# Optimization experiments

Hardware: AMD Instinct MI355X
Metric: run time of the kernel (lower is better)

Reference implementation:

```python
import jax, jax.numpy as jnp
import numpy as np

D_MODEL = 2048
N_HEAD = 16
N_KV_HEAD = 4
D_HEAD = D_MODEL // N_HEAD  # 128
WINDOW = 512
B, T = 2, 2048


def _rope_tables(T, d_head, base=10000.0):
    inv = 1.0 / (base ** (np.arange(0, d_head, 2, dtype=np.float32) / d_head))
    t = np.arange(T, dtype=np.float32)
    freqs = np.outer(t, inv)  # [T, d_head//2]
    return jnp.asarray(np.cos(freqs)), jnp.asarray(np.sin(freqs))


def setup_inputs() -> dict:
    key = jax.random.key(0)
    ks = jax.random.split(key, 5)
    cos, sin = _rope_tables(T, D_HEAD)
    s = 1.0 / np.sqrt(D_MODEL)
    return {
        "x": jax.random.normal(ks[0], (B, T, D_MODEL), jnp.float32),
        "cos": cos,
        "sin": sin,
        "Wq": jax.random.normal(ks[1], (D_MODEL, D_MODEL), jnp.float32) * s,
        "Wk": jax.random.normal(ks[2], (D_MODEL, N_KV_HEAD * D_HEAD), jnp.float32) * s,
        "Wv": jax.random.normal(ks[3], (D_MODEL, N_KV_HEAD * D_HEAD), jnp.float32) * s,
        "Wo": jax.random.normal(ks[4], (D_MODEL, D_MODEL), jnp.float32) * s,
    }


def _apply_rope(t, cos, sin):
    # t: [B, T, H, D]; cos/sin: [T, D//2]; interleaved-pair (complex) rotation
    tr = t[..., 0::2]
    ti = t[..., 1::2]
    c = cos[None, :, None, :]
    s = sin[None, :, None, :]
    out_r = tr * c - ti * s
    out_i = tr * s + ti * c
    return jnp.stack([out_r, out_i], axis=-1).reshape(t.shape)


def reference(x, cos, sin, Wq, Wk, Wv, Wo):
    Bx, Tx, C = x.shape
    q = (x @ Wq).reshape(Bx, Tx, N_HEAD, D_HEAD)       # [B,T,H,D]
    k = (x @ Wk).reshape(Bx, Tx, N_KV_HEAD, D_HEAD)    # [B,T,Hkv,D]
    v = (x @ Wv).reshape(Bx, Tx, N_KV_HEAD, D_HEAD)
    q = _apply_rope(q, cos, sin)
    k = _apply_rope(k, cos, sin)
    n_rep = N_HEAD // N_KV_HEAD
    k = jnp.repeat(k, n_rep, axis=2)  # [B,T,H,D]
    v = jnp.repeat(v, n_rep, axis=2)
    scale = 1.0 / np.sqrt(D_HEAD)
    att = jnp.einsum("bihd,bjhd->bhij", q, k) * scale  # [B,H,T,T]
    i = jnp.arange(Tx)[:, None]
    j = jnp.arange(Tx)[None, :]
    mask = (j <= i) & (j >= i - WINDOW + 1)            # causal sliding window
    att = jnp.where(mask[None, None], att, -jnp.inf)
    att = jax.nn.softmax(att, axis=-1)
    y = jnp.einsum("bhij,bjhd->bihd", att, v).reshape(Bx, Tx, C)
    return y @ Wo
```

## Files before the change

### kernel.cpp

```cpp
#include <hip/hip_runtime.h>
#include <hip/hip_bf16.h>
#include <cstdint>
#include <cstddef>

#define B_ 2
#define T_ 2048
#define NH 16
#define NKV 4
#define DH 128
#define DM 2048
#define WIN 512
#define QKS 2560

typedef __attribute__((ext_vector_type(4))) float f32x4;
typedef __attribute__((ext_vector_type(8))) __bf16 bf16x8;

using bf16 = __hip_bfloat16;

__device__ inline void gload_lds16(const void* g, void* l) {
  __builtin_amdgcn_global_load_lds(
      (const __attribute__((address_space(1))) void*)g,
      (__attribute__((address_space(3))) void*)l, 16, 0, 0);
}

__device__ inline unsigned pack_bf2(float a, float b) {
  unsigned short ua = __builtin_bit_cast(unsigned short, __float2bfloat16(a));
  unsigned short ub = __builtin_bit_cast(unsigned short, __float2bfloat16(b));
  return (unsigned)ua | ((unsigned)ub << 16);
}

#define FBAR()                           \
  do {                                   \
    asm volatile("" ::: "memory");       \
    __builtin_amdgcn_s_barrier();        \
    asm volatile("" ::: "memory");       \
  } while (0)

__global__ __launch_bounds__(256) void k_prep(const float* __restrict__ x,
                                              const float* __restrict__ Wq,
                                              const float* __restrict__ Wk,
                                              const float* __restrict__ Wv,
                                              const float* __restrict__ Wo,
                                              bf16* __restrict__ xb,
                                              bf16* __restrict__ Wqkvt,
                                              bf16* __restrict__ Wot) {
  int id = blockIdx.x;
  int tid = threadIdx.x;
  if (id >= 2560) {
    size_t base = (size_t)(id - 2560) * 4096 + tid * 16;
#pragma unroll
    for (int j = 0; j < 4; ++j) {
      float4 v = *(const float4*)(x + base + j * 4);
      ushort4 o;
      o.x = __builtin_bit_cast(unsigned short, __float2bfloat16(v.x));
      o.y = __builtin_bit_cast(unsigned short, __float2bfloat16(v.y));
      o.z = __builtin_bit_cast(unsigned short, __float2bfloat16(v.z));
      o.w = __builtin_bit_cast(unsigned short, __float2bfloat16(v.w));
      *(ushort4*)(xb + base + j * 4) = o;
    }
    return;
  }
  const float* W;
  bf16* Wt;
  int N, bx, by;
  if (id < 1024) { W = Wq; Wt = Wqkvt; N = 2048; bx = id & 31; by = id >> 5; }
  else if (id < 1280) { id -= 1024; W = Wk; Wt = Wqkvt + (size_t)2048 * 2048; N = 512; bx = id & 7; by = id >> 3; }
  else if (id < 1536) { id -= 1280; W = Wv; Wt = Wqkvt + (size_t)2560 * 2048; N = 512; bx = id & 7; by = id >> 3; }
  else { id -= 1536; W = Wo; Wt = Wot; N = 2048; bx = id & 31; by = id >> 5; }

  __shared__ float tile[64][65];
  int n0 = bx * 64, k0 = by * 64;
  int tx = tid & 63, tg = tid >> 6;
#pragma unroll
  for (int r = 0; r < 16; ++r) {
    int k = tg * 16 + r;
    tile[k][tx] = W[(size_t)(k0 + k) * N + n0 + tx];
  }
  __syncthreads();
#pragma unroll
  for (int r = 0; r < 16; ++r) {
    int nn = tg * 16 + r;
    Wt[(size_t)(n0 + nn) * 2048 + k0 + tx] = __float2bfloat16(tile[tx][nn]);
  }
}

template <int BN, int EPI>
__global__ __launch_bounds__(512, 2) void k_gemm2(const bf16* __restrict__ A,
                                                  const bf16* __restrict__ Bt,
                                                  void* __restrict__ Cout,
                                                  int M, int N, int K,
                                                  const float* __restrict__ cosT,
                                                  const float* __restrict__ sinT,
                                                  bf16* __restrict__ vt) {
  constexpr int NR = BN / 32;
  constexpr int NB = BN * 128 / 8192;
  __shared__ __align__(16) char As_[2][32768];
  __shared__ __align__(16) char Bs_[2][BN * 128];

  const int tid = threadIdx.x;
  const int w = tid >> 6, lane = tid & 63;
  const int li = lane & 15, g = lane >> 4;
  const int wm = w >> 1, wn = w & 1;

  const int nwg = gridDim.x * gridDim.y;
  int bid = blockIdx.y * gridDim.x + blockIdx.x;
  bid = (bid & 7) * (nwg >> 3) + (bid >> 3);
  const int m0 = (bid / gridDim.x) * 256;
  const int n0 = (bid % gridDim.x) * BN;

  const int ntiles = K >> 6;

  auto sA = [&](int buf, int tile, int h, int issue) {
    if (tile >= ntiles) return;
    const int rl = issue * 64 + (tid >> 3);
    const int row = (rl >> 5) * 64 + h * 32 + (rl & 31);
    const int sl = tid & 7;
    const bf16* src = A + (size_t)(m0 + row) * K + tile * 64 + ((sl ^ (rl & 7)) * 8);
    gload_lds16(src, As_[buf] + h * 16384 + issue * 8192 + tid * 16);
  };
  auto sB = [&](int buf, int tile, int issue) {
    if (tile >= ntiles) return;
    const int block = issue * 8 + w;
    const int rr = block * 8 + (lane >> 3);
    const int sl = lane & 7;
    const bf16* src = Bt + (size_t)(n0 + rr) * K + tile * 64 + ((sl ^ (rr & 7)) * 8);
    gload_lds16(src, Bs_[buf] + block * 1024);
  };

  const int swz0 = (g ^ (li & 7)) * 16;
  const int swz1 = ((4 + g) ^ (li & 7)) * 16;
  bf16x8 af[4], bv[NR * 2];
  f32x4 acc[4][NR] = {};

  auto readA = [&](int buf, int mh) {
#pragma unroll
    for (int m2 = 0; m2 < 2; ++m2) {
      const int rl = wm * 32 + m2 * 16 + li;
      const char* p = As_[buf] + mh * 16384 + rl * 128;
      af[m2 * 2 + 0] = *(const bf16x8*)(p + swz0);
      af[m2 * 2 + 1] = *(const bf16x8*)(p + swz1);
    }
  };
  auto readB = [&](int buf) {
#pragma unroll
    for (int n = 0; n < NR; ++n) {
      const char* p = Bs_[buf] + (wn * (NR * 16) + n * 16 + li) * 128;
      bv[n * 2 + 0] = *(const bf16x8*)(p + swz0);
      bv[n * 2 + 1] = *(const bf16x8*)(p + swz1);
    }
  };
  auto MMA = [&](int mh) {
    __builtin_amdgcn_s_setprio(1);
#pragma unroll
    for (int m2 = 0; m2 < 2; ++m2)
#pragma unroll
      for (int n = 0; n < NR; ++n)
#pragma unroll
        for (int kk = 0; kk < 2; ++kk)
          acc[mh * 2 + m2][n] = __builtin_amdgcn_mfma_f32_16x16x32_bf16(
              af[m2 * 2 + kk], bv[n * 2 + kk], acc[mh * 2 + m2][n], 0, 0, 0);
    __builtin_amdgcn_s_setprio(0);
  };

  sA(0, 0, 0, 0); sA(0, 0, 0, 1);
#pragma unroll
  for (int i = 0; i < NB; ++i) sB(0, 0, i);
  sA(0, 0, 1, 0); sA(0, 0, 1, 1);
  asm volatile("s_waitcnt vmcnt(2)" ::: "memory");
  __builtin_amdgcn_sched_barrier(0);
  FBAR();

  for (int t = 0; t < ntiles; ++t) {
    const int cb = t & 1;
    const bool last = (t == ntiles - 1);
    readA(cb, 0); readB(cb);
    sA(cb ^ 1, t + 1, 0, 0); sA(cb ^ 1, t + 1, 0, 1);
#pragma unroll
    for (int i = 0; i < NB; ++i) sB(cb ^ 1, t + 1, i);
    if (last) {
      asm volatile("s_waitcnt vmcnt(0)" ::: "memory");
    } else if constexpr (NB == 3) {
      asm volatile("s_waitcnt vmcnt(5)" ::: "memory");
    } else {
      asm volatile("s_waitcnt vmcnt(4)" ::: "memory");
    }
    __builtin_amdgcn_sched_barrier(0);
    FBAR(); MMA(0); FBAR();
    readA(cb, 1);
    sA(cb ^ 1, t + 1, 1, 0); sA(cb ^ 1, t + 1, 1, 1);
    if (last)
      asm volatile("s_waitcnt vmcnt(0)" ::: "memory");
    else
      asm volatile("s_waitcnt vmcnt(2)" ::: "memory");
    __builtin_amdgcn_sched_barrier(0);
    FBAR(); MMA(1); FBAR();
  }

#pragma unroll
  for (int mf = 0; mf < 4; ++mf)
#pragma unroll
    for (int nf = 0; nf < NR; ++nf) {
      const int colc = n0 + wn * (NR * 16) + nf * 16;
      const int col = colc + li;
      const int row0 = m0 + wm * 64 + mf * 16 + g * 4;
      if constexpr (EPI == 2) {
        if (colc < QKS) {
          const float qs = (colc < 2048) ? 0.08838834764831845f : 1.0f;
          const int i = (col & 127) >> 1;
          const float sgn = (li & 1) ? 1.0f : -1.0f;
#pragma unroll
          for (int r = 0; r < 4; ++r) {
            const int trow = (row0 + r) & (T_ - 1);
            float v = acc[mf][nf][r];
            float pv = __shfl_xor(v, 1);
            float c = cosT[trow * 64 + i], s = sinT[trow * 64 + i];
            float o = (v * c + pv * (sgn * s)) * qs;
            ((bf16*)Cout)[(size_t)(row0 + r) * QKS + col] = __float2bfloat16(o);
          }
        } else {
          unsigned lo = pack_bf2(acc[mf][nf][0], acc[mf][nf][1]);
          unsigned hi = pack_bf2(acc[mf][nf][2], acc[mf][nf][3]);
          uint2 pk = {lo, hi};
          *(uint2*)(vt + (size_t)(col - QKS) * (B_ * T_) + row0) = pk;
        }
      } else {
#pragma unroll
        for (int r = 0; r < 4; ++r)
          ((float*)Cout)[(size_t)(row0 + r) * N + col] = acc[mf][nf][r];
      }
    }
}

__global__ __launch_bounds__(512, 2) void k_attn(const bf16* __restrict__ qkv,
                                                 const bf16* __restrict__ vt,
                                                 bf16* __restrict__ Y) {
  __shared__ __align__(16) char Ks[2][9216];
  __shared__ __align__(16) char Vs[2][10240];
  __shared__ __align__(16) char Pl[8][2][1280];
  const int lane = threadIdx.x & 63;
  const int w = threadIdx.x >> 6;
  const int li = lane & 15, g = lane >> 4;
  const int t0 = ((int)gridDim.x - 1 - (int)blockIdx.x) * 64;
  const int b = blockIdx.y / NKV, kvh = blockIdx.y % NKV;
  const int h = kvh * 4 + (w >> 1);
  const int qrow0 = t0 + (w & 1) * 32;

  bf16x8 qf[2][4];
#pragma unroll
  for (int s = 0; s < 2; ++s) {
    const bf16* qbase = qkv + (size_t)(b * T_ + qrow0 + s * 16 + li) * QKS + h * DH;
#pragma unroll
    for (int dk = 0; dk < 4; ++dk) qf[s][dk] = *(const bf16x8*)(qbase + dk * 32 + g * 8);
  }

  float mrow[2] = {-1e4f, -1e4f};
  float srow[2] = {0.f, 0.f};
  f32x4 acc[2][8] = {};

  int ks0 = t0 - (WIN - 1);
  if (ks0 < 0) ks0 = 0;
  ks0 &= ~31;
  const int nt = (t0 + 63 - ks0) / 32 + 1;

  const bf16* kgbase = qkv + (size_t)(b * T_) * QKS + DM + kvh * DH;
  const bf16* vgbase = vt + (size_t)(kvh * DH) * (B_ * T_) + b * T_;

  auto STAGE = [&](int buf, int kt) {
    for (int c = w; c < 19; c += 8) {
      if (c < 9) {
        int slot = c * 64 + lane;
        int row = slot / 17, cc = slot % 17;
        if (slot >= 544) { row = 0; cc = 0; }
        if (cc == 16) cc = 0;
        const bf16* src = kgbase + (size_t)(kt + row) * QKS + cc * 8;
        gload_lds16(src, Ks[buf] + c * 1024);
      } else {
        int c2 = c - 9;
        int slot = c2 * 64 + lane;
        int row = slot / 5, cc = slot % 5;
        if (cc == 4) cc = 0;
        const bf16* src = vgbase + (size_t)row * (B_ * T_) + kt + cc * 8;
        gload_lds16(src, Vs[buf] + c2 * 1024);
      }
    }
  };

  STAGE(0, ks0);
  __syncthreads();
  int cur = 0;

  for (int it = 0; it < nt; ++it) {
    const int kt = ks0 + it * 32;
    if (it + 1 < nt) STAGE(cur ^ 1, kt + 32);

    if (!(kt > qrow0 + 31 || kt + 31 < qrow0 - (WIN - 1))) {
      f32x4 sc[2][2] = {};
#pragma unroll
      for (int n = 0; n < 2; ++n)
#pragma unroll
        for (int dk = 0; dk < 4; ++dk) {
          bf16x8 kf = *(const bf16x8*)(Ks[cur] + (n * 16 + li) * 272 + dk * 64 + g * 16);
          sc[0][n] = __builtin_amdgcn_mfma_f32_16x16x32_bf16(kf, qf[0][dk], sc[0][n], 0, 0, 0);
          sc[1][n] = __builtin_amdgcn_mfma_f32_16x16x32_bf16(kf, qf[1][dk], sc[1][n], 0, 0, 0);
        }

#pragma unroll
      for (int s = 0; s < 2; ++s) {
        const int t = qrow0 + s * 16 + li;
        float p[2][4];
        float pmax = -1e30f;
#pragma unroll
        for (int n = 0; n < 2; ++n)
#pragma unroll
          for (int r = 0; r < 4; ++r) {
            int key = kt + n * 16 + g * 4 + r;
            bool valid = (key <= t) && (key > t - WIN);
            float pv = valid ? sc[s][n][r] : -1e30f;
            p[n][r] = pv;
            pmax = fmaxf(pmax, pv);
          }
        pmax = fmaxf(pmax, __shfl_xor(pmax, 16));
        pmax = fmaxf(pmax, __shfl_xor(pmax, 32));

        if (!__all(pmax <= mrow[s])) {
          float nm = fmaxf(mrow[s], pmax);
          float alpha = __expf(mrow[s] - nm);
          mrow[s] = nm;
          srow[s] *= alpha;
          float af_[4];
#pragma unroll
          for (int r = 0; r < 4; ++r) af_[r] = __shfl(alpha, (g << 2) + r);
#pragma unroll
          for (int db = 0; db < 8; ++db)
#pragma unroll
            for (int r = 0; r < 4; ++r) acc[s][db][r] *= af_[r];
        }

        float rs = 0.f;
#pragma unroll
        for (int n = 0; n < 2; ++n)
#pragma unroll
          for (int r = 0; r < 4; ++r) {
            p[n][r] = __expf(p[n][r] - mrow[s]);
            rs += p[n][r];
          }
        rs += __shfl_xor(rs, 16);
        rs += __shfl_xor(rs, 32);
        srow[s] += rs;

#pragma unroll
        for (int n = 0; n < 2; ++n) {
          *(unsigned*)(Pl[w][s] + li * 80 + n * 32 + g * 8) = pack_bf2(p[n][0], p[n][1]);
          *(unsigned*)(Pl[w][s] + li * 80 + n * 32 + g * 8 + 4) = pack_bf2(p[n][2], p[n][3]);
        }
      }

      bf16x8 pf0 = *(const bf16x8*)(Pl[w][0] + li * 80 + g * 16);
      bf16x8 pf1 = *(const bf16x8*)(Pl[w][1] + li * 80 + g * 16);
#pragma unroll
      for (int db = 0; db < 8; ++db) {
        bf16x8 vf = *(const bf16x8*)(Vs[cur] + (db * 16 + li) * 80 + g * 16);
        acc[0][db] = __builtin_amdgcn_mfma_f32_16x16x32_bf16(pf0, vf, acc[0][db], 0, 0, 0);
        acc[1][db] = __builtin_amdgcn_mfma_f32_16x16x32_bf16(pf1, vf, acc[1][db], 0, 0, 0);
      }
    }

    __syncthreads();
    cur ^= 1;
  }

#pragma unroll
  for (int s = 0; s < 2; ++s) {
    float inv[4];
#pragma unroll
    for (int r = 0; r < 4; ++r) inv[r] = 1.f / __shfl(srow[s], (g << 2) + r);
    bf16* ybase = Y + (size_t)(b * T_ + qrow0 + s * 16 + (g << 2)) * DM + h * DH;
#pragma unroll
    for (int r = 0; r < 4; ++r)
#pragma unroll
      for (int db = 0; db < 8; ++db)
        ybase[(size_t)r * DM + db * 16 + li] = __float2bfloat16(acc[s][db][r] * inv[r]);
  }
}

extern "C" void kernel_launch(void* const* d_in, const int* in_sizes, int n_in,
                              void* d_out, int out_size, void* d_ws, size_t ws_size,
                              hipStream_t stream) {
  const float* x = (const float*)d_in[0];
  const float* cosT = (const float*)d_in[1];
  const float* sinT = (const float*)d_in[2];
  const float* Wq = (const float*)d_in[3];
  const float* Wk = (const float*)d_in[4];
  const float* Wv = (const float*)d_in[5];
  const float* Wo = (const float*)d_in[6];
  float* out = (float*)d_out;

  char* ws = (char*)d_ws;
  bf16* xb = (bf16*)ws;     ws += (size_t)4096 * 2048 * 2;
  bf16* Wqkvt = (bf16*)ws;  ws += (size_t)3072 * 2048 * 2;
  bf16* Wot = (bf16*)ws;    ws += (size_t)2048 * 2048 * 2;
  bf16* qkv = (bf16*)ws;    ws += (size_t)4096 * QKS * 2;
  bf16* vt = (bf16*)ws;     ws += (size_t)512 * 4096 * 2;
  bf16* yb = xb;

  k_prep<<<4608, 256, 0, stream>>>(x, Wq, Wk, Wv, Wo, xb, Wqkvt, Wot);

  k_gemm2<192, 2><<<dim3(3072 / 192, 4096 / 256), 512, 0, stream>>>(
      xb, Wqkvt, qkv, 4096, 3072, 2048, cosT, sinT, vt);

  k_attn<<<dim3(T_ / 64, B_ * NKV), 512, 0, stream>>>(qkv, vt, yb);

  k_gemm2<128, 0><<<dim3(2048 / 128, 4096 / 256), 512, 0, stream>>>(
      yb, Wot, out, 4096, 2048, 2048, nullptr, nullptr, nullptr);
}
```

Baseline: 161.7 us.

## Remap GEMM warps to a 2x4 grid with 128-row warp tiles

The GEMM changes its warp layout from 4x2 to 2x4, so each warp computes 128 rows by BN/4 columns with eight A fragments and BN/64 B fragments. The A staging address mapping and the register arrays are rewritten to match. This shifts LDS read reuse towards fewer B reads per MMA but doubles the accumulator rows per warp. It may raise register pressure under the 2-blocks-per-SM launch bound. The attention kernel also drops its minimum-blocks launch bound, which frees the compiler's register budget.

```diff
diff --git a/kernel.cpp b/kernel.cpp
--- a/kernel.cpp
+++ b/kernel.cpp
@@ -92,15 +92,14 @@
                                                   const float* __restrict__ cosT,
                                                   const float* __restrict__ sinT,
                                                   bf16* __restrict__ vt) {
-  constexpr int NR = BN / 32;
-  constexpr int NB = BN * 128 / 8192;
+  constexpr int NR = BN / 64;
   __shared__ __align__(16) char As_[2][32768];
   __shared__ __align__(16) char Bs_[2][BN * 128];
 
   const int tid = threadIdx.x;
   const int w = tid >> 6, lane = tid & 63;
   const int li = lane & 15, g = lane >> 4;
-  const int wm = w >> 1, wn = w & 1;
+  const int wm = w >> 2, wn = w & 3;
 
   const int nwg = gridDim.x * gridDim.y;
   int bid = blockIdx.y * gridDim.x + blockIdx.x;
@@ -110,13 +109,13 @@
 
   const int ntiles = K >> 6;
 
-  auto sA = [&](int buf, int tile, int h, int issue) {
+  auto sA = [&](int buf, int tile, int half, int issue) {
     if (tile >= ntiles) return;
-    const int rl = issue * 64 + (tid >> 3);
-    const int row = (rl >> 5) * 64 + h * 32 + (rl & 31);
-    const int sl = tid & 7;
-    const bf16* src = A + (size_t)(m0 + row) * K + tile * 64 + ((sl ^ (rl & 7)) * 8);
-    gload_lds16(src, As_[buf] + h * 16384 + issue * 8192 + tid * 16);
+    const int R0 = half * 64 + issue * 128;
+    const int rr = R0 + w * 8 + (lane >> 3);
+    const int sl = lane & 7;
+    const bf16* src = A + (size_t)(m0 + rr) * K + tile * 64 + ((sl ^ (rr & 7)) * 8);
+    gload_lds16(src, As_[buf] + (R0 + w * 8) * 128);
   };
   auto sB = [&](int buf, int tile, int issue) {
     if (tile >= ntiles) return;
@@ -129,16 +128,15 @@
 
   const int swz0 = (g ^ (li & 7)) * 16;
   const int swz1 = ((4 + g) ^ (li & 7)) * 16;
-  bf16x8 af[4], bv[NR * 2];
-  f32x4 acc[4][NR] = {};
+  bf16x8 af[8], bv[NR * 2];
+  f32x4 acc[8][NR] = {};
 
   auto readA = [&](int buf, int mh) {
 #pragma unroll
-    for (int m2 = 0; m2 < 2; ++m2) {
-      const int rl = wm * 32 + m2 * 16 + li;
-      const char* p = As_[buf] + mh * 16384 + rl * 128;
-      af[m2 * 2 + 0] = *(const bf16x8*)(p + swz0);
-      af[m2 * 2 + 1] = *(const bf16x8*)(p + swz1);
+    for (int m = 0; m < 4; ++m) {
+      const char* p = As_[buf] + (wm * 128 + mh * 64 + m * 16 + li) * 128;
+      af[m * 2 + 0] = *(const bf16x8*)(p + swz0);
+      af[m * 2 + 1] = *(const bf16x8*)(p + swz1);
     }
   };
   auto readB = [&](int buf) {
@@ -152,19 +150,35 @@
   auto MMA = [&](int mh) {
     __builtin_amdgcn_s_setprio(1);
 #pragma unroll
-    for (int m2 = 0; m2 < 2; ++m2)
+    for (int m = 0; m < 4; ++m)
 #pragma unroll
       for (int n = 0; n < NR; ++n)
 #pragma unroll
         for (int kk = 0; kk < 2; ++kk)
-          acc[mh * 2 + m2][n] = __builtin_amdgcn_mfma_f32_16x16x32_bf16(
-              af[m2 * 2 + kk], bv[n * 2 + kk], acc[mh * 2 + m2][n], 0, 0, 0);
+          acc[mh * 4 + m][n] = __builtin_amdgcn_mfma_f32_16x16x32_bf16(
+              af[m * 2 + kk], bv[n * 2 + kk], acc[mh * 4 + m][n], 0, 0, 0);
     __builtin_amdgcn_s_setprio(0);
   };
+  auto VMWA = [&](bool last) {
+    if (last)
+      asm volatile("s_waitcnt vmcnt(0)" ::: "memory");
+    else if constexpr (NR == 3)
+      asm volatile("s_waitcnt vmcnt(5)" ::: "memory");
+    else
+      asm volatile("s_waitcnt vmcnt(4)" ::: "memory");
+    __builtin_amdgcn_sched_barrier(0);
+  };
+  auto VMWB = [&](bool last) {
+    if (last)
+      asm volatile("s_waitcnt vmcnt(0)" ::: "memory");
+    else
+      asm volatile("s_waitcnt vmcnt(2)" ::: "memory");
+    __builtin_amdgcn_sched_barrier(0);
+  };
 
   sA(0, 0, 0, 0); sA(0, 0, 0, 1);
 #pragma unroll
-  for (int i = 0; i < NB; ++i) sB(0, 0, i);
+  for (int i = 0; i < NR; ++i) sB(0, 0, i);
   sA(0, 0, 1, 0); sA(0, 0, 1, 1);
   asm volatile("s_waitcnt vmcnt(2)" ::: "memory");
   __builtin_amdgcn_sched_barrier(0);
@@ -176,33 +190,22 @@
     readA(cb, 0); readB(cb);
     sA(cb ^ 1, t + 1, 0, 0); sA(cb ^ 1, t + 1, 0, 1);
 #pragma unroll
-    for (int i = 0; i < NB; ++i) sB(cb ^ 1, t + 1, i);
-    if (last) {
-      asm volatile("s_waitcnt vmcnt(0)" ::: "memory");
-    } else if constexpr (NB == 3) {
-      asm volatile("s_waitcnt vmcnt(5)" ::: "memory");
-    } else {
-      asm volatile("s_waitcnt vmcnt(4)" ::: "memory");
-    }
-    __builtin_amdgcn_sched_barrier(0);
+    for (int i = 0; i < NR; ++i) sB(cb ^ 1, t + 1, i);
+    VMWA(last);
     FBAR(); MMA(0); FBAR();
     readA(cb, 1);
     sA(cb ^ 1, t + 1, 1, 0); sA(cb ^ 1, t + 1, 1, 1);
-    if (last)
-      asm volatile("s_waitcnt vmcnt(0)" ::: "memory");
-    else
-      asm volatile("s_waitcnt vmcnt(2)" ::: "memory");
-    __builtin_amdgcn_sched_barrier(0);
+    VMWB(last);
     FBAR(); MMA(1); FBAR();
   }
 
 #pragma unroll
-  for (int mf = 0; mf < 4; ++mf)
+  for (int mf = 0; mf < 8; ++mf)
 #pragma unroll
     for (int nf = 0; nf < NR; ++nf) {
       const int colc = n0 + wn * (NR * 16) + nf * 16;
       const int col = colc + li;
-      const int row0 = m0 + wm * 64 + mf * 16 + g * 4;
+      const int row0 = m0 + wm * 128 + mf * 16 + g * 4;
       if constexpr (EPI == 2) {
         if (colc < QKS) {
           const float qs = (colc < 2048) ? 0.08838834764831845f : 1.0f;
@@ -231,9 +234,9 @@
     }
 }
 
-__global__ __launch_bounds__(512, 2) void k_attn(const bf16* __restrict__ qkv,
-                                                 const bf16* __restrict__ vt,
-                                                 bf16* __restrict__ Y) {
+__global__ __launch_bounds__(512) void k_attn(const bf16* __restrict__ qkv,
+                                              const bf16* __restrict__ vt,
+                                              bf16* __restrict__ Y) {
   __shared__ __align__(16) char Ks[2][9216];
   __shared__ __align__(16) char Vs[2][10240];
   __shared__ __align__(16) char Pl[8][2][1280];
```

After: 161.2 us. About the same (-0.3%).
